# Kernel optimization log

Measured on AMD Instinct MI355X. Metric: run time of the kernel, lower is better.

The kernel has to match this reference:

```python
import jax, jax.numpy as jnp
import numpy as np

R_SOFTPLUS_0 = 1.442695041  # 1/softplus(0) = 1/ln(2)
NEG_INF = -1e9


def setup_inputs() -> dict:
    key = jax.random.key(0)
    ks = jax.random.split(key, 6)
    B, L, E, H = 16, 1024, 512, 8
    Dh = E // H
    return {
        "x": jax.random.normal(ks[0], (B, L, E), jnp.float32),
        "in_proj_weight": jax.random.normal(ks[1], (3 * E, E), jnp.float32) * (E ** -0.5),
        "in_proj_bias": jax.random.normal(ks[2], (3 * E,), jnp.float32) * 0.02,
        "out_proj_weight": jax.random.normal(ks[3], (E, E), jnp.float32) * (E ** -0.5),
        "out_proj_bias": jax.random.normal(ks[4], (E,), jnp.float32) * 0.02,
        "qs_scale": jnp.zeros((Dh,), jnp.float32),  # init.zeros in QueryScaler
        "key_padding_mask": jnp.zeros((B, L), jnp.bool_),  # True = ignore key
    }


def reference(x, in_proj_weight, in_proj_bias, out_proj_weight, out_proj_bias,
              qs_scale, key_padding_mask):
    B, L, E = x.shape
    Dh = qs_scale.shape[0]
    H = E // Dh
    # packed in-projection: q,k,v = x @ W^T + b, split along last dim
    qkv = jnp.einsum("ble,fe->blf", x, in_proj_weight) + in_proj_bias
    q, k, v = jnp.split(qkv, 3, axis=-1)
    q = q.reshape(B, L, H, Dh)
    k = k.reshape(B, L, H, Dh)
    v = v.reshape(B, L, H, Dh)
    # QueryScaler: per-head-dim learned softplus scale on projected q
    q = q * (R_SOFTPLUS_0 * jax.nn.softplus(qs_scale))
    # scaled dot-product attention
    scores = jnp.einsum("blhd,bshd->bhls", q, k) / jnp.sqrt(jnp.asarray(Dh, q.dtype))
    scores = jnp.where(key_padding_mask[:, None, None, :], NEG_INF, scores)
    probs = jax.nn.softmax(scores, axis=-1)
    out = jnp.einsum("bhls,bshd->blhd", probs, v).reshape(B, L, E)
    # output projection
    return jnp.einsum("ble,fe->blf", out, out_proj_weight) + out_proj_bias
```

## Files before the change

### kernel.cpp

```cpp
#include <hip/hip_runtime.h>
#include <hip/hip_bf16.h>
#include <math.h>

#define B_ 16
#define L_ 1024
#define E_ 512
#define H_ 8
#define DH 64

typedef unsigned short u16;
typedef __attribute__((ext_vector_type(8))) short bf16x8;
typedef __attribute__((ext_vector_type(8))) unsigned short u16x8;
typedef __attribute__((ext_vector_type(4))) float f32x4;
typedef __attribute__((ext_vector_type(16))) float f32x16;

#define MFMA16(A, B, C) __builtin_amdgcn_mfma_f32_16x16x32_bf16(A, B, C, 0, 0, 0)
#define MFMA32(A, B, C) __builtin_amdgcn_mfma_f32_32x32x16_bf16(A, B, C, 0, 0, 0)

#if __has_builtin(__builtin_amdgcn_exp2f)
#define EXP2(x) __builtin_amdgcn_exp2f(x)
#else
#define EXP2(x) exp2f(x)
#endif

__device__ inline u16 f2b(float x) {
    __hip_bfloat16 h = __float2bfloat16(x);
    u16 u; __builtin_memcpy(&u, &h, 2); return u;
}

__device__ inline unsigned int cvt_pk_bf16(float a, float b) {
    unsigned int r;
    asm("v_cvt_pk_bf16_f32 %0, %1, %2" : "=v"(r) : "v"(a), "v"(b));
    return r;
}

__global__ void qscale_kernel(const float* __restrict__ qs_scale,
                              float* __restrict__ qscale) {
    int d = threadIdx.x;
    if (d < DH) {
        float x = qs_scale[d];
        float sp = (x > 20.f) ? x : log1pf(expf(x));
        qscale[d] = 1.442695041f * sp * 0.125f * 1.442695041f;
    }
}

__global__ __launch_bounds__(256) void cvt_bf16(
    const float* __restrict__ x, const float* __restrict__ wi,
    const float* __restrict__ wo, u16* __restrict__ xb,
    u16* __restrict__ wib, u16* __restrict__ wob)
{
    int i = blockIdx.x * 256 + threadIdx.x;
    const float* src; u16* dst; size_t off;
    if (i < 1048576)      { src = x;  dst = xb;  off = (size_t)i * 8; }
    else if (i < 1146880) { src = wi; dst = wib; off = (size_t)(i - 1048576) * 8; }
    else                  { src = wo; dst = wob; off = (size_t)(i - 1146880) * 8; }
    float4 a = *(const float4*)(src + off);
    float4 b = *(const float4*)(src + off + 4);
    u16x8 r;
    r[0] = f2b(a.x); r[1] = f2b(a.y); r[2] = f2b(a.z); r[3] = f2b(a.w);
    r[4] = f2b(b.x); r[5] = f2b(b.y); r[6] = f2b(b.z); r[7] = f2b(b.w);
    *(u16x8*)(dst + off) = r;
}

template<int MODE>
__global__ __launch_bounds__(256) void gemm_bf16(
    const u16* __restrict__ A, const u16* __restrict__ W,
    const float* __restrict__ bias, const float* __restrict__ qscale,
    float* __restrict__ Dout, u16* __restrict__ Qb, u16* __restrict__ Kb,
    u16* __restrict__ Vtb)
{
    __shared__ u16 sA[2][4096];
    __shared__ u16 sB[2][4096];
    const int tid = threadIdx.x;
    const int m0 = blockIdx.x * 128;
    const int n0 = blockIdx.y * 128;
    const int wid = tid >> 6, lane = tid & 63;
    const int g = lane >> 4, c = lane & 15;
    const int wr = wid >> 1, wc = wid & 1;

    const int arow = tid >> 2;
    const int swg = (arow & 3) ^ ((arow >> 2) & 3);
    const int ch = (tid & 3) ^ swg;
    const u16* Asrc = A + (size_t)(m0 + arow) * 512 + ch * 8;
    const u16* Bsrc = W + (size_t)(n0 + arow) * 512 + ch * 8;

    auto stage = [&](int nbuf, int ks) {
        const int k0 = ks * 32;
        __builtin_amdgcn_global_load_lds(
            (const __attribute__((address_space(1))) unsigned int*)(Asrc + k0),
            (__attribute__((address_space(3))) unsigned int*)&sA[nbuf][wid * 512], 16, 0, 0);
        __builtin_amdgcn_global_load_lds(
            (const __attribute__((address_space(1))) unsigned int*)(Asrc + (size_t)64 * 512 + k0),
            (__attribute__((address_space(3))) unsigned int*)&sA[nbuf][2048 + wid * 512], 16, 0, 0);
        __builtin_amdgcn_global_load_lds(
            (const __attribute__((address_space(1))) unsigned int*)(Bsrc + k0),
            (__attribute__((address_space(3))) unsigned int*)&sB[nbuf][wid * 512], 16, 0, 0);
        __builtin_amdgcn_global_load_lds(
            (const __attribute__((address_space(1))) unsigned int*)(Bsrc + (size_t)64 * 512 + k0),
            (__attribute__((address_space(3))) unsigned int*)&sB[nbuf][2048 + wid * 512], 16, 0, 0);
    };

    f32x4 acc[4][4];
    #pragma unroll
    for (int m = 0; m < 4; m++)
        #pragma unroll
        for (int n = 0; n < 4; n++) acc[m][n] = (f32x4){0.f, 0.f, 0.f, 0.f};

    const int swr = (c & 3) ^ ((c >> 2) & 3);
    const int chA = (g ^ swr) * 8;

    stage(0, 0);
    #pragma unroll 1
    for (int ks = 0; ks < 16; ks++) {
        const int cur = ks & 1;
        asm volatile("s_waitcnt vmcnt(0) lgkmcnt(0)" ::: "memory");
        __syncthreads();
        if (ks < 15) stage(cur ^ 1, ks + 1);

        bf16x8 af[4], bfr[4];
        #pragma unroll
        for (int m = 0; m < 4; m++)
            af[m] = *(const bf16x8*)&sA[cur][(wr * 64 + m * 16 + c) * 32 + chA];
        #pragma unroll
        for (int n = 0; n < 4; n++)
            bfr[n] = *(const bf16x8*)&sB[cur][(wc * 64 + n * 16 + c) * 32 + chA];
        #pragma unroll
        for (int m = 0; m < 4; m++)
            #pragma unroll
            for (int n = 0; n < 4; n++)
                acc[m][n] = MFMA16(af[m], bfr[n], acc[m][n]);
    }

    #pragma unroll
    for (int m = 0; m < 4; m++) {
        int rbase = m0 + wr * 64 + m * 16 + 4 * g;
        #pragma unroll
        for (int n = 0; n < 4; n++) {
            int f = n0 + wc * 64 + n * 16 + c;
            f32x4 v = acc[m][n];
            float bv = bias[f];
            if (MODE == 1) {
                #pragma unroll
                for (int reg = 0; reg < 4; reg++)
                    Dout[(size_t)(rbase + reg) * E_ + f] = v[reg] + bv;
            } else {
                int part = f >> 9, w = f & 511, h = w >> 6, d = w & 63;
                int bb = rbase >> 10;
                int l0 = rbase & 1023;
                size_t bh = (size_t)(bb * H_ + h);
                if (part == 0) {
                    float qs = qscale[d];
                    #pragma unroll
                    for (int reg = 0; reg < 4; reg++)
                        Qb[(bh * L_ + l0 + reg) * DH + d] = f2b((v[reg] + bv) * qs);
                } else if (part == 1) {
                    #pragma unroll
                    for (int reg = 0; reg < 4; reg++)
                        Kb[(bh * L_ + l0 + reg) * DH + d] = f2b(v[reg] + bv);
                } else {
                    ushort4 pk;
                    pk.x = f2b(v[0] + bv); pk.y = f2b(v[1] + bv);
                    pk.z = f2b(v[2] + bv); pk.w = f2b(v[3] + bv);
                    *(ushort4*)(Vtb + (bh * DH + d) * L_ + l0) = pk;
                }
            }
        }
    }
}

__global__ __launch_bounds__(256, 4) void attn_mfma(
    const u16* __restrict__ Q, const u16* __restrict__ K,
    const u16* __restrict__ Vt, const unsigned char* __restrict__ mask,
    u16* __restrict__ O)
{
    __shared__ u16 Kbuf[2][2048];
    __shared__ u16 Vbuf[2][2048];
    __shared__ u16 P_lds[4][32][36];

    const int bid = blockIdx.x;
    const int w = (bid & 7) * 128 + (bid >> 3);
    const int bh = w >> 3;
    const int blk = w & 7;
    const int tid = threadIdx.x;
    const int wid = tid >> 6;
    const int q0 = blk * 128 + wid * 32;
    const int b = bh >> 3;
    const int h = bh & (H_ - 1);

    const int lane = tid & 63;
    const int c = lane & 31;
    const int hi = lane >> 5;

    const u16* Qp = Q + ((size_t)bh * L_ + q0) * DH;
    const u16* Kp = K + (size_t)bh * L_ * DH;
    const u16* Vp = Vt + (size_t)bh * DH * L_;
    const unsigned char* mp = mask + (size_t)b * L_;

    const int krow = tid >> 3, kch = (tid & 7) ^ (krow & 7);
    const int vrow = tid >> 2, vch = (tid & 3) ^ ((vrow & 3) ^ ((vrow >> 2) & 3));
    const u16* Kg = Kp + (size_t)krow * DH + kch * 8;
    const u16* Vg = Vp + (size_t)vrow * L_ + vch * 8;

    auto stage = [&](int nbuf, int kt) {
        __builtin_amdgcn_global_load_lds(
            (const __attribute__((address_space(1))) unsigned int*)(Kg + (size_t)kt * DH),
            (__attribute__((address_space(3))) unsigned int*)&Kbuf[nbuf][wid * 512],
            16, 0, 0);
        __builtin_amdgcn_global_load_lds(
            (const __attribute__((address_space(1))) unsigned int*)(Vg + kt),
            (__attribute__((address_space(3))) unsigned int*)&Vbuf[nbuf][wid * 512],
            16, 0, 0);
    };

    unsigned int mor = 0;
    {
        const unsigned int* mp32 = (const unsigned int*)mp;
        #pragma unroll
        for (int i = 0; i < 4; i++) mor |= mp32[lane + i * 64];
    }
    const bool anyMask = (__ballot(mor != 0) != 0ULL);

    stage(0, 0);

    bf16x8 qf[4];
    #pragma unroll
    for (int s2 = 0; s2 < 4; s2++)
        qf[s2] = *(const bf16x8*)(Qp + c * DH + s2 * 16 + hi * 8);

    f32x16 oacc0 = {}, oacc1 = {};
    float mrun = -INFINITY, lrun = 0.f;

    int kslot[4];
    #pragma unroll
    for (int s2 = 0; s2 < 4; s2++)
        kslot[s2] = (c * 8 + (((2 * s2 + hi)) ^ (c & 7))) * 8;
    const int swzv = (c & 3) ^ ((c >> 2) & 3);
    int vslot[2][2];
    #pragma unroll
    for (int dt = 0; dt < 2; dt++)
        #pragma unroll
        for (int s = 0; s < 2; s++)
            vslot[dt][s] = ((dt * 32 + c) * 4 + (((2 * s + hi)) ^ swzv)) * 8;

    #pragma unroll 1
    for (int t = 0; t < 32; ++t) {
        const int cur = t & 1;
        const int kt = t * 32;
        asm volatile("s_waitcnt vmcnt(0) lgkmcnt(0)" ::: "memory");
        __syncthreads();

        bf16x8 kf[4];
        #pragma unroll
        for (int s2 = 0; s2 < 4; s2++)
            kf[s2] = *(const bf16x8*)&Kbuf[cur][kslot[s2]];
        bf16x8 vf[2][2];
        #pragma unroll
        for (int dt = 0; dt < 2; dt++)
            #pragma unroll
            for (int s = 0; s < 2; s++)
                vf[dt][s] = *(const bf16x8*)&Vbuf[cur][vslot[dt][s]];

        if (t < 31) stage(cur ^ 1, kt + 32);

        f32x16 st = {};
        #pragma unroll
        for (int s2 = 0; s2 < 4; s2++)
            st = MFMA32(kf[s2], qf[s2], st);

        if (anyMask) {
            #pragma unroll
            for (int r = 0; r < 16; r++) {
                int key = kt + (r & 3) + 8 * (r >> 2) + 4 * hi;
                if (mp[key]) st[r] = -1e9f;
            }
        }

        float m01 = fmaxf(st[0], st[1]),  m23 = fmaxf(st[2], st[3]);
        float m45 = fmaxf(st[4], st[5]),  m67 = fmaxf(st[6], st[7]);
        float m89 = fmaxf(st[8], st[9]),  mab = fmaxf(st[10], st[11]);
        float mcd = fmaxf(st[12], st[13]), mef = fmaxf(st[14], st[15]);
        float tm = fmaxf(fmaxf(fmaxf(m01, m23), fmaxf(m45, m67)),
                         fmaxf(fmaxf(m89, mab), fmaxf(mcd, mef)));
        tm = fmaxf(tm, __shfl_xor(tm, 32));

        if (!__all(tm <= mrun + 8.f)) {
            float mnew = fmaxf(mrun, tm);
            float corr = EXP2(mrun - mnew);
            lrun *= corr;
            #pragma unroll
            for (int r = 0; r < 16; r++) {
                int row = (r & 3) + 8 * (r >> 2) + 4 * hi;
                float cr = __shfl(corr, row);
                oacc0[r] *= cr;
                oacc1[r] *= cr;
            }
            mrun = mnew;
        }

        float p[16];
        #pragma unroll
        for (int r = 0; r < 16; r++) p[r] = EXP2(st[r] - mrun);
        float s01 = (p[0] + p[1]) + (p[2] + p[3]);
        float s23 = (p[4] + p[5]) + (p[6] + p[7]);
        float s45 = (p[8] + p[9]) + (p[10] + p[11]);
        float s67 = (p[12] + p[13]) + (p[14] + p[15]);
        float ls = (s01 + s23) + (s45 + s67);
        ls += __shfl_xor(ls, 32);
        lrun += ls;

        #pragma unroll
        for (int rp = 0; rp < 4; rp++) {
            uint2 pw;
            pw.x = cvt_pk_bf16(p[4 * rp], p[4 * rp + 1]);
            pw.y = cvt_pk_bf16(p[4 * rp + 2], p[4 * rp + 3]);
            *(uint2*)(&P_lds[wid][c][8 * rp + 4 * hi]) = pw;
        }
        asm volatile("s_waitcnt lgkmcnt(0)" ::: "memory");
        __builtin_amdgcn_sched_barrier(0);
        bf16x8 pa0 = *(const bf16x8*)(&P_lds[wid][c][hi * 8]);
        bf16x8 pa1 = *(const bf16x8*)(&P_lds[wid][c][16 + hi * 8]);
        asm volatile("" ::: "memory");

        oacc0 = MFMA32(pa0, vf[0][0], oacc0);
        oacc0 = MFMA32(pa1, vf[0][1], oacc0);
        oacc1 = MFMA32(pa0, vf[1][0], oacc1);
        oacc1 = MFMA32(pa1, vf[1][1], oacc1);
    }

    #pragma unroll
    for (int r = 0; r < 16; r++) {
        int row = (r & 3) + 8 * (r >> 2) + 4 * hi;
        float lq = __shfl(lrun, row);
        float inv = 1.f / lq;
        size_t base = ((size_t)(b * L_ + q0 + row)) * E_ + h * DH + c;
        O[base] = f2b(oacc0[r] * inv);
        O[base + 32] = f2b(oacc1[r] * inv);
    }
}

extern "C" void kernel_launch(void* const* d_in, const int* in_sizes, int n_in,
                              void* d_out, int out_size, void* d_ws, size_t ws_size,
                              hipStream_t stream) {
    const float* x     = (const float*)d_in[0];
    const float* w_in  = (const float*)d_in[1];
    const float* b_in  = (const float*)d_in[2];
    const float* w_out = (const float*)d_in[3];
    const float* b_out = (const float*)d_in[4];
    const float* qs    = (const float*)d_in[5];
    const unsigned char* mask = (const unsigned char*)d_in[6];
    float* out = (float*)d_out;

    char* base = (char*)d_ws;
    const size_t NELEM = (size_t)B_ * L_ * E_;
    float* qscale = (float*)base;
    u16* xb  = (u16*)(base + 256);
    u16* wib = xb + NELEM;
    u16* wob = wib + 786432;
    u16* Qb  = wob + 262144;
    u16* Kb  = Qb + NELEM;
    u16* Vtb = Kb + NELEM;
    u16* Ob  = Vtb + NELEM;

    qscale_kernel<<<1, 64, 0, stream>>>(qs, qscale);
    cvt_bf16<<<4608, 256, 0, stream>>>(x, w_in, w_out, xb, wib, wob);
    gemm_bf16<0><<<dim3(128, 12), 256, 0, stream>>>(
        xb, wib, b_in, qscale, nullptr, Qb, Kb, Vtb);
    attn_mfma<<<dim3(1024), 256, 0, stream>>>(Qb, Kb, Vtb, mask, Ob);
    gemm_bf16<1><<<dim3(128, 4), 256, 0, stream>>>(
        Ob, wob, b_out, nullptr, out, nullptr, nullptr, nullptr);
}
```

Baseline: 130.4 us.

## Triple-buffer K/V tiles in attention and fold qscale into convert kernel

The attention kernel moves from double to triple buffering of K/V tiles in LDS. It prefetches two tiles ahead and waits only for the oldest outstanding loads (vmcnt(2)) instead of draining all global loads every iteration. The separate qscale launch is merged into the bf16 conversion kernel, which removes one kernel launch. The extra LDS per block may reduce occupancy, and removing the post-load wait relies on correct vmcnt accounting.

```diff
diff --git a/kernel.cpp b/kernel.cpp
--- a/kernel.cpp
+++ b/kernel.cpp
@@ -34,21 +34,17 @@
     return r;
 }
 
-__global__ void qscale_kernel(const float* __restrict__ qs_scale,
-                              float* __restrict__ qscale) {
-    int d = threadIdx.x;
-    if (d < DH) {
-        float x = qs_scale[d];
-        float sp = (x > 20.f) ? x : log1pf(expf(x));
-        qscale[d] = 1.442695041f * sp * 0.125f * 1.442695041f;
-    }
-}
-
 __global__ __launch_bounds__(256) void cvt_bf16(
     const float* __restrict__ x, const float* __restrict__ wi,
-    const float* __restrict__ wo, u16* __restrict__ xb,
-    u16* __restrict__ wib, u16* __restrict__ wob)
+    const float* __restrict__ wo, const float* __restrict__ qs_scale,
+    u16* __restrict__ xb, u16* __restrict__ wib, u16* __restrict__ wob,
+    float* __restrict__ qscale)
 {
+    if (blockIdx.x == 0 && threadIdx.x < DH) {
+        float s = qs_scale[threadIdx.x];
+        float sp = (s > 20.f) ? s : log1pf(expf(s));
+        qscale[threadIdx.x] = 1.442695041f * sp * 0.125f * 1.442695041f;
+    }
     int i = blockIdx.x * 256 + threadIdx.x;
     const float* src; u16* dst; size_t off;
     if (i < 1048576)      { src = x;  dst = xb;  off = (size_t)i * 8; }
@@ -173,8 +169,8 @@
     const u16* __restrict__ Vt, const unsigned char* __restrict__ mask,
     u16* __restrict__ O)
 {
-    __shared__ u16 Kbuf[2][2048];
-    __shared__ u16 Vbuf[2][2048];
+    __shared__ u16 Kbuf[3][2048];
+    __shared__ u16 Vbuf[3][2048];
     __shared__ u16 P_lds[4][32][36];
 
     const int bid = blockIdx.x;
@@ -220,12 +216,13 @@
     }
     const bool anyMask = (__ballot(mor != 0) != 0ULL);
 
-    stage(0, 0);
-
     bf16x8 qf[4];
     #pragma unroll
     for (int s2 = 0; s2 < 4; s2++)
         qf[s2] = *(const bf16x8*)(Qp + c * DH + s2 * 16 + hi * 8);
+
+    stage(0, 0);
+    stage(1, 32);
 
     f32x16 oacc0 = {}, oacc1 = {};
     float mrun = -INFINITY, lrun = 0.f;
@@ -244,10 +241,12 @@
 
     #pragma unroll 1
     for (int t = 0; t < 32; ++t) {
-        const int cur = t & 1;
+        const int cur = t % 3;
         const int kt = t * 32;
-        asm volatile("s_waitcnt vmcnt(0) lgkmcnt(0)" ::: "memory");
-        __syncthreads();
+        if (t < 31) { asm volatile("s_waitcnt vmcnt(2) lgkmcnt(0)" ::: "memory"); }
+        else        { asm volatile("s_waitcnt vmcnt(0) lgkmcnt(0)" ::: "memory"); }
+        __builtin_amdgcn_s_barrier();
+        asm volatile("" ::: "memory");
 
         bf16x8 kf[4];
         #pragma unroll
@@ -260,7 +259,7 @@
             for (int s = 0; s < 2; s++)
                 vf[dt][s] = *(const bf16x8*)&Vbuf[cur][vslot[dt][s]];
 
-        if (t < 31) stage(cur ^ 1, kt + 32);
+        if (t < 30) stage((t + 2) % 3, kt + 64);
 
         f32x16 st = {};
         #pragma unroll
@@ -361,8 +360,7 @@
     u16* Vtb = Kb + NELEM;
     u16* Ob  = Vtb + NELEM;
 
-    qscale_kernel<<<1, 64, 0, stream>>>(qs, qscale);
-    cvt_bf16<<<4608, 256, 0, stream>>>(x, w_in, w_out, xb, wib, wob);
+    cvt_bf16<<<4608, 256, 0, stream>>>(x, w_in, w_out, qs, xb, wib, wob, qscale);
     gemm_bf16<0><<<dim3(128, 12), 256, 0, stream>>>(
         xb, wib, b_in, qscale, nullptr, Qb, Kb, Vtb);
     attn_mfma<<<dim3(1024), 256, 0, stream>>>(Qb, Kb, Vtb, mask, Ob);
```

After: 126.0 us. -3.4%, faster.
